# Optimization experiments

Hardware: AMD Instinct MI355X
Metric: run time of the kernel (lower is better)

Reference implementation:

```python
import jax, jax.numpy as jnp
import numpy as np

N_NODES = 50000
N_EDGES = 800000
NUM_GRAPHS = 256
IN = 128
HID = 256
NUM_CLASSES = 10
EPS = 1e-5


def _glorot(key, shape):
    fan_in, fan_out = shape[0], shape[1]
    lim = (6.0 / (fan_in + fan_out)) ** 0.5
    return jax.random.uniform(key, shape, jnp.float32, -lim, lim)


def setup_inputs() -> dict:
    key = jax.random.key(0)
    ks = jax.random.split(key, 32)
    x = jax.random.normal(ks[0], (N_NODES, IN), jnp.float32)
    edge_index = jax.random.randint(ks[1], (2, N_EDGES), 0, N_NODES, jnp.int64)
    batch = jnp.sort(jax.random.randint(ks[2], (N_NODES,), 0, NUM_GRAPHS, jnp.int64))
    h = IN // 2  # 64
    p = {
        "x": x, "edge_index": edge_index, "batch": batch,
        # SAGEConv: out = lin_l(mean_aggr(x_j)) + lin_r(x_i); lin_l has bias, lin_r none
        "W1l": _glorot(ks[3], (IN, h)), "b1l": jnp.zeros((h,), jnp.float32), "W1r": _glorot(ks[4], (IN, h)),
        "W2l": _glorot(ks[5], (h, h)), "b2l": jnp.zeros((h,), jnp.float32), "W2r": _glorot(ks[6], (h, h)),
        "W3l": _glorot(ks[7], (h, h)), "b3l": jnp.zeros((h,), jnp.float32), "W3r": _glorot(ks[8], (h, h)),
        "lin1_w": _glorot(ks[9], (h, HID)), "lin1_b": jnp.zeros((HID,), jnp.float32),
        "g1": jnp.ones((HID,), jnp.float32), "be1": jnp.zeros((HID,), jnp.float32),
        "lin2_w": _glorot(ks[10], (HID, HID // 2)), "lin2_b": jnp.zeros((HID // 2,), jnp.float32),
        "g2": jnp.ones((HID // 2,), jnp.float32), "be2": jnp.zeros((HID // 2,), jnp.float32),
        "lin3_w": _glorot(ks[11], (HID // 2, HID // 4)), "lin3_b": jnp.zeros((HID // 4,), jnp.float32),
        "g3": jnp.ones((HID // 4,), jnp.float32), "be3": jnp.zeros((HID // 4,), jnp.float32),
        "lin4_w": _glorot(ks[12], (HID // 4, NUM_CLASSES)), "lin4_b": jnp.zeros((NUM_CLASSES,), jnp.float32),
    }
    return p


def sage_conv(x, src, dst, Wl, bl, Wr):
    # mean aggregation of source-node messages at destination nodes
    msg = x[src]  # [E, d] gather
    agg = jax.ops.segment_sum(msg, dst, num_segments=N_NODES)
    cnt = jax.ops.segment_sum(jnp.ones((src.shape[0],), x.dtype), dst, num_segments=N_NODES)
    agg = agg / jnp.maximum(cnt, 1.0)[:, None]
    return agg @ Wl + bl + x @ Wr


def batch_norm(x, gamma, beta):
    # training-mode BN (batch statistics, biased variance) as in torch default
    mean = jnp.mean(x, axis=0)
    var = jnp.mean((x - mean) ** 2, axis=0)
    return (x - mean) / jnp.sqrt(var + EPS) * gamma + beta


def reference(x, edge_index, batch,
              W1l, b1l, W1r, W2l, b2l, W2r, W3l, b3l, W3r,
              lin1_w, lin1_b, g1, be1, lin2_w, lin2_b, g2, be2,
              lin3_w, lin3_b, g3, be3, lin4_w, lin4_b):
    src, dst = edge_index[0], edge_index[1]
    h = sage_conv(x, src, dst, W1l, b1l, W1r)
    h = sage_conv(h, src, dst, W2l, b2l, W2r)
    h = sage_conv(h, src, dst, W3l, b3l, W3r)
    # global_mean_pool over graphs
    s = jax.ops.segment_sum(h, batch, num_segments=NUM_GRAPHS)
    n = jax.ops.segment_sum(jnp.ones((h.shape[0],), h.dtype), batch, num_segments=NUM_GRAPHS)
    c = s / jnp.maximum(n, 1.0)[:, None]
    # dropout is identity (self.training = False)
    c = jnp.tanh(batch_norm(c @ lin1_w + lin1_b, g1, be1))
    c = jnp.tanh(batch_norm(c @ lin2_w + lin2_b, g2, be2))
    c = jnp.tanh(batch_norm(c @ lin3_w + lin3_b, g3, be3))
    return c @ lin4_w + lin4_b
```

## Files before the change

kernel.cpp:

```cpp
#include <hip/hip_runtime.h>
#include <hip/hip_bf16.h>

#define N_NODES   50000
#define N_EDGES   800000
#define NUM_GRAPHS 256
#define IN_DIM    128
#define HD        64
#define EPS       1e-5f
#define SCAN_NB   196
#define NB_HEAD   64

typedef __hip_bfloat16 bf16;

__global__ void k_diag(float* __restrict__ out, int n, float v) {
    int t = blockIdx.x * 256 + threadIdx.x;
    if (t < n) out[t] = v;
}

__global__ void k_count(const int* __restrict__ dst, const int* __restrict__ batch,
                        int* __restrict__ cnti, int* __restrict__ pos,
                        int* __restrict__ gb) {
    int e = blockIdx.x * 256 + threadIdx.x;
    if (e < N_EDGES) pos[e] = atomicAdd(&cnti[dst[e]], 1);
    if (e < N_NODES) {
        int bg = batch[e];
        int bnext = (e + 1 < N_NODES) ? batch[e + 1] : NUM_GRAPHS;
        if (e == 0) {
            for (int g = 0; g <= bg; ++g) gb[g] = 0;
        }
        for (int g = bg + 1; g <= bnext; ++g) gb[g] = e + 1;
    }
}

__global__ void k_scan1(const int* __restrict__ cnti, int* __restrict__ off,
                        int* __restrict__ bsum) {
    __shared__ int wsum[4];
    int idx = blockIdx.x * 256 + threadIdx.x;
    int lane = threadIdx.x & 63, wid = threadIdx.x >> 6;
    int v = (idx < N_NODES) ? cnti[idx] : 0;
    int s = v;
    #pragma unroll
    for (int o = 1; o < 64; o <<= 1) {
        int u = __shfl_up(s, o);
        if (lane >= o) s += u;
    }
    if (lane == 63) wsum[wid] = s;
    __syncthreads();
    int wbase = 0;
    #pragma unroll
    for (int w = 0; w < 4; w++) wbase += (w < wid) ? wsum[w] : 0;
    if (idx < N_NODES) off[idx] = wbase + s - v;
    if (threadIdx.x == 255) bsum[blockIdx.x] = wbase + s;
}

__global__ void k_scan3(int* __restrict__ off, const int* __restrict__ bsum,
                        const int* __restrict__ gb, float* __restrict__ invc) {
    __shared__ int wsum[4];
    __shared__ int spre;
    int lane = threadIdx.x & 63, wid = threadIdx.x >> 6;
    int v = (threadIdx.x < blockIdx.x) ? bsum[threadIdx.x] : 0;
    #pragma unroll
    for (int o = 32; o > 0; o >>= 1) v += __shfl_down(v, o);
    if (lane == 0) wsum[wid] = v;
    __syncthreads();
    if (threadIdx.x == 0) spre = wsum[0] + wsum[1] + wsum[2] + wsum[3];
    __syncthreads();
    int pre = spre;
    int idx = blockIdx.x * 256 + threadIdx.x;
    if (idx < N_NODES) off[idx] += pre;
    else if (idx == N_NODES) off[N_NODES] = N_EDGES;
    if (blockIdx.x == 0 && threadIdx.x < NUM_GRAPHS) {
        int c0 = gb[threadIdx.x], c1 = gb[threadIdx.x + 1];
        invc[threadIdx.x] = 1.0f / (float)max(c1 - c0, 1);
    }
}

__global__ void k_fill(const int* __restrict__ src, const int* __restrict__ dst,
                       const int* __restrict__ off, const int* __restrict__ pos,
                       int* __restrict__ nbr) {
    int e = blockIdx.x * 256 + threadIdx.x;
    if (e >= N_EDGES) return;
    int d = dst[e];
    nbr[off[d] + pos[e]] = src[e];
}

template <int K, int NB>
__global__ __launch_bounds__(256) void k_xform3(
        const float* __restrict__ X, const float* __restrict__ Wl,
        const float* __restrict__ Wr, const float* __restrict__ bl,
        bf16* __restrict__ B, float* __restrict__ C) {
    __shared__ float tile[NB * K];
    const int NPW = NB / 4;
    int nodes0 = blockIdx.x * NB;
    {
        const int total4 = NB * K / 4;
        int nmax4 = (N_NODES - nodes0) * K / 4;
        const float4* Xg = (const float4*)(X + (long)nodes0 * K);
        float4* tg = (float4*)tile;
        for (int idx = threadIdx.x; idx < total4; idx += 256) {
            float4 v = make_float4(0.f, 0.f, 0.f, 0.f);
            if (idx < nmax4) v = Xg[idx];
            tg[idx] = v;
        }
    }
    __syncthreads();
    int wave = threadIdx.x >> 6, j = threadIdx.x & 63;
    long base = (long)nodes0 + wave * NPW;
    if (base >= N_NODES) return;
    float accB[NPW], accC[NPW];
    #pragma unroll
    for (int n = 0; n < NPW; n++) { accB[n] = 0.f; accC[n] = 0.f; }
    const float* Xs = tile + (wave * NPW) * K;
    for (int kc = 0; kc < K; kc += 4) {
        float wl0 = Wl[(kc + 0) * HD + j], wr0 = Wr[(kc + 0) * HD + j];
        float wl1 = Wl[(kc + 1) * HD + j], wr1 = Wr[(kc + 1) * HD + j];
        float wl2 = Wl[(kc + 2) * HD + j], wr2 = Wr[(kc + 2) * HD + j];
        float wl3 = Wl[(kc + 3) * HD + j], wr3 = Wr[(kc + 3) * HD + j];
        #pragma unroll
        for (int n = 0; n < NPW; n++) {
            float4 xv = *(const float4*)(Xs + n * K + kc);
            accB[n] = fmaf(xv.x, wl0, accB[n]);
            accC[n] = fmaf(xv.x, wr0, accC[n]);
            accB[n] = fmaf(xv.y, wl1, accB[n]);
            accC[n] = fmaf(xv.y, wr1, accC[n]);
            accB[n] = fmaf(xv.z, wl2, accB[n]);
            accC[n] = fmaf(xv.z, wr2, accC[n]);
            accB[n] = fmaf(xv.w, wl3, accB[n]);
            accC[n] = fmaf(xv.w, wr3, accC[n]);
        }
    }
    float bb = bl[j];
    int nact = (int)min((long)NPW, (long)N_NODES - base);
    for (int n = 0; n < nact; n++) {
        long i = base + n;
        B[i * HD + j] = __float2bfloat16(accB[n]);
        C[i * HD + j] = accC[n] + bb;
    }
}

__device__ __forceinline__ float bflo(unsigned u) { return __uint_as_float(u << 16); }
__device__ __forceinline__ float bfhi(unsigned u) { return __uint_as_float(u & 0xffff0000u); }

template <bool LAST>
__global__ void k_gather(const int* __restrict__ off, const int* __restrict__ nbr,
                         const bf16* __restrict__ Bm, float* __restrict__ C,
                         const int* __restrict__ batch, const float* __restrict__ invc,
                         float* __restrict__ cb) {
    int t = blockIdx.x * 256 + threadIdx.x;
    int i = t >> 6, lane = t & 63;
    if (!LAST && i >= N_NODES) return;
    int q = lane >> 4, c2 = lane & 15;
    int wid = threadIdx.x >> 6;
    const uint2* B2 = (const uint2*)Bm;
    int beg = off[i], end = off[i + 1];
    float4 a0 = make_float4(0.f, 0.f, 0.f, 0.f);
    float4 a1 = make_float4(0.f, 0.f, 0.f, 0.f);
    float4 a2 = make_float4(0.f, 0.f, 0.f, 0.f);
    float4 a3 = make_float4(0.f, 0.f, 0.f, 0.f);
    for (int base = beg; base < end; base += 64) {
        int idx = base + lane;
        int nv = (idx < end) ? nbr[idx] : 0;
        int m = min(64, end - base);
        int tt = 0;
        for (; tt + 16 <= m; tt += 16) {
            int n0 = __shfl(nv, tt + 0 + q);
            int n1 = __shfl(nv, tt + 4 + q);
            int n2 = __shfl(nv, tt + 8 + q);
            int n3 = __shfl(nv, tt + 12 + q);
            uint2 u0 = B2[(long)n0 * 16 + c2];
            uint2 u1 = B2[(long)n1 * 16 + c2];
            uint2 u2 = B2[(long)n2 * 16 + c2];
            uint2 u3 = B2[(long)n3 * 16 + c2];
            a0.x += bflo(u0.x); a0.y += bfhi(u0.x); a0.z += bflo(u0.y); a0.w += bfhi(u0.y);
            a1.x += bflo(u1.x); a1.y += bfhi(u1.x); a1.z += bflo(u1.y); a1.w += bfhi(u1.y);
            a2.x += bflo(u2.x); a2.y += bfhi(u2.x); a2.z += bflo(u2.y); a2.w += bfhi(u2.y);
            a3.x += bflo(u3.x); a3.y += bfhi(u3.x); a3.z += bflo(u3.y); a3.w += bfhi(u3.y);
        }
        for (; tt < m; tt += 4) {
            int n0 = __shfl(nv, tt + q);
            if (tt + q < m) {
                uint2 u0 = B2[(long)n0 * 16 + c2];
                a0.x += bflo(u0.x); a0.y += bfhi(u0.x);
                a0.z += bflo(u0.y); a0.w += bfhi(u0.y);
            }
        }
    }
    float4 s;
    s.x = (a0.x + a1.x) + (a2.x + a3.x);
    s.y = (a0.y + a1.y) + (a2.y + a3.y);
    s.z = (a0.z + a1.z) + (a2.z + a3.z);
    s.w = (a0.w + a1.w) + (a2.w + a3.w);
    s.x += __shfl_xor(s.x, 16); s.x += __shfl_xor(s.x, 32);
    s.y += __shfl_xor(s.y, 16); s.y += __shfl_xor(s.y, 32);
    s.z += __shfl_xor(s.z, 16); s.z += __shfl_xor(s.z, 32);
    s.w += __shfl_xor(s.w, 16); s.w += __shfl_xor(s.w, 32);
    if (!LAST) {
        if (lane < 16) {
            int deg = end - beg;
            float inv = 1.0f / (float)max(deg, 1);
            float4* Cp = (float4*)(C + (long)i * HD + 4 * lane);
            float4 cur = *Cp;
            cur.x += s.x * inv;
            cur.y += s.y * inv;
            cur.z += s.z * inv;
            cur.w += s.w * inv;
            *Cp = cur;
        }
    } else {
        __shared__ float red[4][64];
        __shared__ int gid[4];
        if (lane < 16) {
            int deg = end - beg;
            float inv = 1.0f / (float)max(deg, 1);
            const float4 cur = *(const float4*)(C + (long)i * HD + 4 * lane);
            red[wid][4 * lane + 0] = cur.x + s.x * inv;
            red[wid][4 * lane + 1] = cur.y + s.y * inv;
            red[wid][4 * lane + 2] = cur.z + s.z * inv;
            red[wid][4 * lane + 3] = cur.w + s.w * inv;
        }
        if (lane == 0) gid[wid] = batch[i];
        __syncthreads();
        if (wid == 0) {
            int g0 = gid[0], g1 = gid[1], g2 = gid[2], g3 = gid[3];
            float v0 = red[0][lane], v1 = red[1][lane];
            float v2 = red[2][lane], v3 = red[3][lane];
            if (g0 == g3) {
                atomicAdd(&cb[g0 * HD + lane],
                          ((v0 + v1) + (v2 + v3)) * invc[g0]);
            } else {
                atomicAdd(&cb[g0 * HD + lane], v0 * invc[g0]);
                atomicAdd(&cb[g1 * HD + lane], v1 * invc[g1]);
                atomicAdd(&cb[g2 * HD + lane], v2 * invc[g2]);
                atomicAdd(&cb[g3 * HD + lane], v3 * invc[g3]);
            }
        }
    }
}

__device__ __forceinline__ void gbar(int* bar, int round) {
    __syncthreads();
    if (threadIdx.x == 0) {
        __hip_atomic_fetch_add(bar, 1, __ATOMIC_ACQ_REL, __HIP_MEMORY_SCOPE_AGENT);
        int target = round * NB_HEAD;
        while (__hip_atomic_load(bar, __ATOMIC_ACQUIRE, __HIP_MEMORY_SCOPE_AGENT) < target) {}
    }
    __syncthreads();
}

__device__ __forceinline__ float ag_load(const float* p) {
    return __hip_atomic_load(p, __ATOMIC_RELAXED, __HIP_MEMORY_SCOPE_AGENT);
}

template <int NF>
__device__ __forceinline__ void stage4(float* __restrict__ s, const float* __restrict__ g) {
    const float4* g4 = (const float4*)g;
    float4* s4 = (float4*)s;
    #pragma unroll
    for (int i = 0; i < NF / 1024; i++)
        s4[i * 256 + threadIdx.x] = g4[i * 256 + threadIdx.x];
}

__global__ __launch_bounds__(256) void k_head(
        int* bar, float* __restrict__ gstat,
        const float* __restrict__ l1w, const float* __restrict__ l1b,
        const float* __restrict__ g1, const float* __restrict__ be1,
        const float* __restrict__ l2w, const float* __restrict__ l2b,
        const float* __restrict__ g2, const float* __restrict__ be2,
        const float* __restrict__ l3w, const float* __restrict__ l3b,
        const float* __restrict__ g3, const float* __restrict__ be3,
        const float* __restrict__ w4, const float* __restrict__ b4,
        const float* __restrict__ cb, float* __restrict__ out) {
    __shared__ float WB[32768];
    __shared__ float A1[4][64];
    __shared__ float A2[4][256];
    __shared__ float A3[4][128];
    __shared__ float M3[4][64];
    __shared__ float W4[640];
    float* gs1 = gstat;
    float* gq1 = gstat + 256;
    float* gs2 = gstat + 512;
    float* gq2 = gstat + 640;
    float* gs3 = gstat + 768;
    float* gq3 = gstat + 832;
    int t = threadIdx.x;
    int r0 = blockIdx.x * 4;

    {
        int r = t >> 6, lane = t & 63;
        A1[r][lane] = cb[(r0 + r) * HD + lane];
    }
    if (t < 160) ((float4*)W4)[t] = ((const float4*)w4)[t];
    stage4<16384>(WB + 16384, l1w);
    __syncthreads();

    float v1[4];
    {
        float bj = l1b[t];
        v1[0] = bj; v1[1] = bj; v1[2] = bj; v1[3] = bj;
        const float* Wp = WB + 16384;
        #pragma unroll 16
        for (int k = 0; k < 64; k++) {
            float w = Wp[k * 256 + t];
            v1[0] = fmaf(A1[0][k], w, v1[0]);
            v1[1] = fmaf(A1[1][k], w, v1[1]);
            v1[2] = fmaf(A1[2][k], w, v1[2]);
            v1[3] = fmaf(A1[3][k], w, v1[3]);
        }
        float s = (v1[0] + v1[1]) + (v1[2] + v1[3]);
        float q = (v1[0] * v1[0] + v1[1] * v1[1]) + (v1[2] * v1[2] + v1[3] * v1[3]);
        atomicAdd(&gs1[t], s);
        atomicAdd(&gq1[t], q);
    }
    __syncthreads();
    stage4<32768>(WB, l2w);
    gbar(bar, 1);
    {
        float S = ag_load(&gs1[t]), Q = ag_load(&gq1[t]);
        float mean = S * (1.0f / NUM_GRAPHS);
        float var = Q * (1.0f / NUM_GRAPHS) - mean * mean;
        float sc = rsqrtf(fmaxf(var, 0.f) + EPS) * g1[t];
        float sh = be1[t];
        #pragma unroll
        for (int r = 0; r < 4; r++)
            A2[r][t] = tanhf((v1[r] - mean) * sc + sh);
    }
    __syncthreads();

    float v2[2];
    int j2 = t & 127, rq2 = t >> 7;
    {
        float bj = l2b[j2];
        v2[0] = bj; v2[1] = bj;
        const float* a0 = A2[2 * rq2 + 0];
        const float* a1 = A2[2 * rq2 + 1];
        #pragma unroll 16
        for (int k = 0; k < 256; k++) {
            float w = WB[k * 128 + j2];
            v2[0] = fmaf(a0[k], w, v2[0]);
            v2[1] = fmaf(a1[k], w, v2[1]);
        }
        atomicAdd(&gs2[j2], v2[0] + v2[1]);
        atomicAdd(&gq2[j2], v2[0] * v2[0] + v2[1] * v2[1]);
    }
    __syncthreads();
    stage4<8192>(WB, l3w);
    gbar(bar, 2);
    {
        float S = ag_load(&gs2[j2]), Q = ag_load(&gq2[j2]);
        float mean = S * (1.0f / NUM_GRAPHS);
        float var = Q * (1.0f / NUM_GRAPHS) - mean * mean;
        float sc = rsqrtf(fmaxf(var, 0.f) + EPS) * g2[j2];
        float sh = be2[j2];
        A3[2 * rq2 + 0][j2] = tanhf((v2[0] - mean) * sc + sh);
        A3[2 * rq2 + 1][j2] = tanhf((v2[1] - mean) * sc + sh);
    }
    __syncthreads();

    float v3;
    int j3 = t & 63, rq3 = t >> 6;
    {
        float bj = l3b[j3];
        v3 = bj;
        const float* a = A3[rq3];
        #pragma unroll 16
        for (int k = 0; k < 128; k++) {
            float w = WB[k * 64 + j3];
            v3 = fmaf(a[k], w, v3);
        }
        atomicAdd(&gs3[j3], v3);
        atomicAdd(&gq3[j3], v3 * v3);
    }
    gbar(bar, 3);
    {
        float S = ag_load(&gs3[j3]), Q = ag_load(&gq3[j3]);
        float mean = S * (1.0f / NUM_GRAPHS);
        float var = Q * (1.0f / NUM_GRAPHS) - mean * mean;
        float sc = rsqrtf(fmaxf(var, 0.f) + EPS) * g3[j3];
        float sh = be3[j3];
        M3[rq3][j3] = tanhf((v3 - mean) * sc + sh);
    }
    __syncthreads();

    if (t < 40) {
        int q = t / 10, jf = t % 10;
        const float* rp = M3[q];
        float s = b4[jf];
        #pragma unroll
        for (int k = 0; k < 64; k++) s = fmaf(rp[k], W4[k * 10 + jf], s);
        out[(r0 + q) * 10 + jf] = s;
    }
}

extern "C" void kernel_launch(void* const* d_in, const int* in_sizes, int n_in,
                              void* d_out, int out_size, void* d_ws, size_t ws_size,
                              hipStream_t stream) {
    const float* x     = (const float*)d_in[0];
    const int*   ei    = (const int*) d_in[1];
    const int*   batch = (const int*) d_in[2];
    const float *W1l = (const float*)d_in[3],  *b1l = (const float*)d_in[4],  *W1r = (const float*)d_in[5];
    const float *W2l = (const float*)d_in[6],  *b2l = (const float*)d_in[7],  *W2r = (const float*)d_in[8];
    const float *W3l = (const float*)d_in[9],  *b3l = (const float*)d_in[10], *W3r = (const float*)d_in[11];
    const float *lin1_w = (const float*)d_in[12], *lin1_b = (const float*)d_in[13];
    const float *g1 = (const float*)d_in[14], *be1 = (const float*)d_in[15];
    const float *lin2_w = (const float*)d_in[16], *lin2_b = (const float*)d_in[17];
    const float *g2 = (const float*)d_in[18], *be2 = (const float*)d_in[19];
    const float *lin3_w = (const float*)d_in[20], *lin3_b = (const float*)d_in[21];
    const float *g3 = (const float*)d_in[22], *be3 = (const float*)d_in[23];
    const float *lin4_w = (const float*)d_in[24], *lin4_b = (const float*)d_in[25];

    const int* srcp = ei;
    const int* dstp = ei + N_EDGES;

    const long NF = (long)N_NODES * HD;
    char* wsb  = (char*)d_ws;
    int*  cnti = (int*)wsb;
    int*  bar  = cnti + 50048;
    float* gstat = (float*)(bar + 8);
    int*  pos  = (int*)(gstat + 896);
    int*  off  = pos  + 800000;
    int*  nbr  = off  + 50056;
    int*  bsum = nbr  + 800000;
    int*  gb   = bsum + 256;
    float* invc = (float*)(gb + 264);
    bf16* B    = (bf16*)(invc + 256);
    float* H1  = (float*)(B + NF);
    float* H2  = H1  + NF;
    float* cb  = H2  + NF;
    float* endp= cb  + NUM_GRAPHS * HD;

    const size_t NEED = (size_t)((char*)endp - wsb);
    if (ws_size < NEED) {
        k_diag<<<(out_size + 255) / 256, 256, 0, stream>>>((float*)d_out, out_size,
                                                           (float)(ws_size >> 20));
        return;
    }

    const int TB = 256;
    const int gNE = (N_EDGES + TB - 1) / TB;
    const int gNF = (int)((NF + TB - 1) / TB);
    const int gX16 = (N_NODES + 15) / 16;

    hipMemsetAsync(cnti, 0, (50048 + 8 + 896) * sizeof(int), stream);
    hipMemsetAsync(cb, 0, NUM_GRAPHS * HD * sizeof(float), stream);

    k_count<<<gNE, TB, 0, stream>>>(dstp, batch, cnti, pos, gb);
    k_scan1<<<SCAN_NB, TB, 0, stream>>>(cnti, off, bsum);
    k_scan3<<<SCAN_NB, TB, 0, stream>>>(off, bsum, gb, invc);
    k_fill<<<gNE, TB, 0, stream>>>(srcp, dstp, off, pos, nbr);

    k_xform3<IN_DIM, 16><<<gX16, TB, 0, stream>>>(x, W1l, W1r, b1l, B, H1);
    k_gather<false><<<gNF, TB, 0, stream>>>(off, nbr, B, H1, batch, invc, cb);
    k_xform3<HD, 16><<<gX16, TB, 0, stream>>>(H1, W2l, W2r, b2l, B, H2);
    k_gather<false><<<gNF, TB, 0, stream>>>(off, nbr, B, H2, batch, invc, cb);
    k_xform3<HD, 16><<<gX16, TB, 0, stream>>>(H2, W3l, W3r, b3l, B, H1);
    k_gather<true><<<gNF, TB, 0, stream>>>(off, nbr, B, H1, batch, invc, cb);

    k_head<<<NB_HEAD, TB, 0, stream>>>(bar, gstat,
                                       lin1_w, lin1_b, g1, be1,
                                       lin2_w, lin2_b, g2, be2,
                                       lin3_w, lin3_b, g3, be3,
                                       lin4_w, lin4_b,
                                       cb, (float*)d_out);
}
```

Measured before the change: 359.1 us.

## Fuse next-layer SAGE linear transform into gather epilogue

The neighbor-mean gather kernel now finishes the current layer's output row in shared memory. In the same kernel it immediately applies the next layer's Wl/Wr transform, so the standalone transform kernels for layers 2 and 3 disappear and the intermediate hidden activations are no longer written and re-read. Node CSR bounds are precomputed as an int2 array while filling the neighbor list. B buffers are ping-ponged and C is updated in place per row. Each lane now does a 64-step matvec reading the weights from global/cache, which adds per-node arithmetic and weight loads to the latency-bound gather.

```diff
diff --git a/kernel.cpp b/kernel.cpp
--- a/kernel.cpp
+++ b/kernel.cpp
@@ -77,8 +77,9 @@
 
 __global__ void k_fill(const int* __restrict__ src, const int* __restrict__ dst,
                        const int* __restrict__ off, const int* __restrict__ pos,
-                       int* __restrict__ nbr) {
+                       int* __restrict__ nbr, int2* __restrict__ bounds) {
     int e = blockIdx.x * 256 + threadIdx.x;
+    if (e < N_NODES) bounds[e] = make_int2(off[e], off[e + 1]);
     if (e >= N_EDGES) return;
     int d = dst[e];
     nbr[off[d] + pos[e]] = src[e];
@@ -142,17 +143,21 @@
 __device__ __forceinline__ float bfhi(unsigned u) { return __uint_as_float(u & 0xffff0000u); }
 
 template <bool LAST>
-__global__ void k_gather(const int* __restrict__ off, const int* __restrict__ nbr,
-                         const bf16* __restrict__ Bm, float* __restrict__ C,
-                         const int* __restrict__ batch, const float* __restrict__ invc,
-                         float* __restrict__ cb) {
+__global__ __launch_bounds__(256) void k_gx(
+        const int2* __restrict__ bounds, const int* __restrict__ nbr,
+        const bf16* __restrict__ Bin, const float* __restrict__ Cin,
+        const float* __restrict__ Wl, const float* __restrict__ Wr,
+        const float* __restrict__ bl,
+        bf16* __restrict__ Bout, float* __restrict__ Cout,
+        const int* __restrict__ batch, const float* __restrict__ invc,
+        float* __restrict__ cb) {
     int t = blockIdx.x * 256 + threadIdx.x;
     int i = t >> 6, lane = t & 63;
-    if (!LAST && i >= N_NODES) return;
     int q = lane >> 4, c2 = lane & 15;
     int wid = threadIdx.x >> 6;
-    const uint2* B2 = (const uint2*)Bm;
-    int beg = off[i], end = off[i + 1];
+    const uint2* B2 = (const uint2*)Bin;
+    int2 be = bounds[i];
+    int beg = be.x, end = be.y;
     float4 a0 = make_float4(0.f, 0.f, 0.f, 0.f);
     float4 a1 = make_float4(0.f, 0.f, 0.f, 0.f);
     float4 a2 = make_float4(0.f, 0.f, 0.f, 0.f);
@@ -194,30 +199,32 @@
     s.y += __shfl_xor(s.y, 16); s.y += __shfl_xor(s.y, 32);
     s.z += __shfl_xor(s.z, 16); s.z += __shfl_xor(s.z, 32);
     s.w += __shfl_xor(s.w, 16); s.w += __shfl_xor(s.w, 32);
+    int deg = end - beg;
+    float inv = 1.0f / (float)max(deg, 1);
+    const float4 cur = *(const float4*)(Cin + (long)i * HD + 4 * c2);
+    float4 h4;
+    h4.x = cur.x + s.x * inv;
+    h4.y = cur.y + s.y * inv;
+    h4.z = cur.z + s.z * inv;
+    h4.w = cur.w + s.w * inv;
     if (!LAST) {
-        if (lane < 16) {
-            int deg = end - beg;
-            float inv = 1.0f / (float)max(deg, 1);
-            float4* Cp = (float4*)(C + (long)i * HD + 4 * lane);
-            float4 cur = *Cp;
-            cur.x += s.x * inv;
-            cur.y += s.y * inv;
-            cur.z += s.z * inv;
-            cur.w += s.w * inv;
-            *Cp = cur;
-        }
+        __shared__ float hrow[4][64];
+        if (lane < 16) *(float4*)&hrow[wid][4 * c2] = h4;
+        __syncthreads();
+        float aB = 0.f, aC = bl[lane];
+        const float* hp = hrow[wid];
+        #pragma unroll 8
+        for (int k = 0; k < 64; k++) {
+            float hk = hp[k];
+            aB = fmaf(hk, Wl[k * HD + lane], aB);
+            aC = fmaf(hk, Wr[k * HD + lane], aC);
+        }
+        Bout[(long)i * HD + lane] = __float2bfloat16(aB);
+        Cout[(long)i * HD + lane] = aC;
     } else {
         __shared__ float red[4][64];
         __shared__ int gid[4];
-        if (lane < 16) {
-            int deg = end - beg;
-            float inv = 1.0f / (float)max(deg, 1);
-            const float4 cur = *(const float4*)(C + (long)i * HD + 4 * lane);
-            red[wid][4 * lane + 0] = cur.x + s.x * inv;
-            red[wid][4 * lane + 1] = cur.y + s.y * inv;
-            red[wid][4 * lane + 2] = cur.z + s.z * inv;
-            red[wid][4 * lane + 3] = cur.w + s.w * inv;
-        }
+        if (lane < 16) *(float4*)&red[wid][4 * c2] = h4;
         if (lane == 0) gid[wid] = batch[i];
         __syncthreads();
         if (wid == 0) {
@@ -422,11 +429,12 @@
     int*  bsum = nbr  + 800000;
     int*  gb   = bsum + 256;
     float* invc = (float*)(gb + 264);
-    bf16* B    = (bf16*)(invc + 256);
-    float* H1  = (float*)(B + NF);
-    float* H2  = H1  + NF;
-    float* cb  = H2  + NF;
-    float* endp= cb  + NUM_GRAPHS * HD;
+    int2* bounds = (int2*)(invc + 256);
+    bf16* Ba   = (bf16*)(bounds + 50000);
+    bf16* Bb   = Ba + NF;
+    float* C   = (float*)(Bb + NF);
+    float* cb  = C + NF;
+    float* endp= cb + NUM_GRAPHS * HD;
 
     const size_t NEED = (size_t)((char*)endp - wsb);
     if (ws_size < NEED) {
@@ -446,14 +454,15 @@
     k_count<<<gNE, TB, 0, stream>>>(dstp, batch, cnti, pos, gb);
     k_scan1<<<SCAN_NB, TB, 0, stream>>>(cnti, off, bsum);
     k_scan3<<<SCAN_NB, TB, 0, stream>>>(off, bsum, gb, invc);
-    k_fill<<<gNE, TB, 0, stream>>>(srcp, dstp, off, pos, nbr);
-
-    k_xform3<IN_DIM, 16><<<gX16, TB, 0, stream>>>(x, W1l, W1r, b1l, B, H1);
-    k_gather<false><<<gNF, TB, 0, stream>>>(off, nbr, B, H1, batch, invc, cb);
-    k_xform3<HD, 16><<<gX16, TB, 0, stream>>>(H1, W2l, W2r, b2l, B, H2);
-    k_gather<false><<<gNF, TB, 0, stream>>>(off, nbr, B, H2, batch, invc, cb);
-    k_xform3<HD, 16><<<gX16, TB, 0, stream>>>(H2, W3l, W3r, b3l, B, H1);
-    k_gather<true><<<gNF, TB, 0, stream>>>(off, nbr, B, H1, batch, invc, cb);
+    k_fill<<<gNE, TB, 0, stream>>>(srcp, dstp, off, pos, nbr, bounds);
+
+    k_xform3<IN_DIM, 16><<<gX16, TB, 0, stream>>>(x, W1l, W1r, b1l, Ba, C);
+    k_gx<false><<<gNF, TB, 0, stream>>>(bounds, nbr, Ba, C, W2l, W2r, b2l,
+                                        Bb, C, batch, invc, cb);
+    k_gx<false><<<gNF, TB, 0, stream>>>(bounds, nbr, Bb, C, W3l, W3r, b3l,
+                                        Ba, C, batch, invc, cb);
+    k_gx<true><<<gNF, TB, 0, stream>>>(bounds, nbr, Ba, C, W3l, W3r, b3l,
+                                       Bb, C, batch, invc, cb);
 
     k_head<<<NB_HEAD, TB, 0, stream>>>(bar, gstat,
                                        lin1_w, lin1_b, g1, be1,
```

Result: slower. 390.9 us (+8.9%).
